# Optimization experiments

Hardware: AMD Instinct MI355X
Metric: run time of the kernel (lower is better)

Reference implementation:

```python
import jax, jax.numpy as jnp
import numpy as np

D_IN = 1024
D_OUT = 1024
NUM_HEAD = 16
HEAD_DIM = D_OUT // NUM_HEAD
CTX = 2048


def setup_inputs() -> dict:
    key = jax.random.key(0)
    ks = jax.random.split(key, 7)
    s = 0.02
    x = jax.random.normal(ks[0], (2, CTX, D_IN), dtype=jnp.float32)
    Wq = jax.random.normal(ks[1], (D_IN, D_OUT), dtype=jnp.float32) * s
    Wk = jax.random.normal(ks[2], (D_IN, D_OUT), dtype=jnp.float32) * s
    Wv = jax.random.normal(ks[3], (D_IN, D_OUT), dtype=jnp.float32) * s
    Wo = jax.random.normal(ks[4], (D_OUT, D_OUT), dtype=jnp.float32) * s
    bo = jax.random.normal(ks[5], (D_OUT,), dtype=jnp.float32) * s
    return {"x": x, "Wq": Wq, "Wk": Wk, "Wv": Wv, "Wo": Wo, "bo": bo}


def reference(x, Wq, Wk, Wv, Wo, bo):
    B, T, _ = x.shape
    # QKV projections, split into heads: [B, H, T, hd]
    def split_heads(y):
        return y.reshape(B, T, NUM_HEAD, HEAD_DIM).transpose(0, 2, 1, 3)
    q = split_heads(x @ Wq)
    k = split_heads(x @ Wk)
    v = split_heads(x @ Wv)
    # scaled causal attention scores [B, H, T, T]
    scores = jnp.einsum("bhqd,bhkd->bhqk", q, k) / jnp.sqrt(
        jnp.asarray(HEAD_DIM, dtype=x.dtype))
    causal = jnp.tril(jnp.ones((T, T), dtype=bool))  # mask buffer triu(diag=1) -> keep lower tri
    scores = jnp.where(causal[None, None], scores, jnp.asarray(-jnp.inf, dtype=x.dtype))
    attn = jax.nn.softmax(scores, axis=-1)
    # dropout with droprate=0.0 is identity
    ctx = jnp.einsum("bhqk,bhkd->bhqd", attn, v)
    ctx = ctx.transpose(0, 2, 1, 3).reshape(B, T, D_OUT)
    return ctx @ Wo + bo
```

## Files before the change

### kernel.cpp

```cpp
#include <hip/hip_runtime.h>

typedef __bf16 bf16x8 __attribute__((ext_vector_type(8)));
typedef float f32x4 __attribute__((ext_vector_type(4)));

__device__ inline float bf2f(unsigned short u) {
    unsigned int x = ((unsigned int)u) << 16;
    return __builtin_bit_cast(float, x);
}
__device__ inline unsigned short f2bf(float f) {
    unsigned int x = __builtin_bit_cast(unsigned int, f);
    x += 0x7fff + ((x >> 16) & 1);
    return (unsigned short)(x >> 16);
}

__device__ __forceinline__ void gl_lds16(const unsigned short* g, unsigned short* l)
{
    __builtin_amdgcn_global_load_lds(
        (const __attribute__((address_space(1))) void*)g,
        (__attribute__((address_space(3))) void*)l, 16, 0, 0);
}

__global__ __launch_bounds__(256)
void prep(const float* __restrict__ x, unsigned short* __restrict__ xb,
          const float* __restrict__ Wq, const float* __restrict__ Wk,
          const float* __restrict__ Wv, unsigned short* __restrict__ wT)
{
    __shared__ unsigned short T[64][72];
    if (blockIdx.x < 2048) {
        const size_t i = ((size_t)blockIdx.x * 256 + threadIdx.x) * 8;
        float4 a = *reinterpret_cast<const float4*>(x + i);
        float4 b = *reinterpret_cast<const float4*>(x + i + 4);
        unsigned short t[8] = { f2bf(a.x), f2bf(a.y), f2bf(a.z), f2bf(a.w),
                                f2bf(b.x), f2bf(b.y), f2bf(b.z), f2bf(b.w) };
        *reinterpret_cast<uint4*>(xb + i) = *reinterpret_cast<uint4*>(t);
        return;
    }
    const int blk = blockIdx.x - 2048;
    const int z = blk >> 8, within = blk & 255;
    const float* W = (z == 0) ? Wq : (z == 1) ? Wk : Wv;
    unsigned short* dstBase = wT + (size_t)z * 1024 * 1024;
    const int k0 = (within >> 4) * 64, n0 = (within & 15) * 64;
    const int r = threadIdx.x >> 2, c0 = (threadIdx.x & 3) * 16;
    const float* src = W + (size_t)(k0 + r) * 1024 + n0 + c0;
    #pragma unroll
    for (int j = 0; j < 16; j += 4) {
        float4 f = *reinterpret_cast<const float4*>(src + j);
        T[r][c0 + j]     = f2bf(f.x);
        T[r][c0 + j + 1] = f2bf(f.y);
        T[r][c0 + j + 2] = f2bf(f.z);
        T[r][c0 + j + 3] = f2bf(f.w);
    }
    __syncthreads();
    unsigned short* dst = dstBase + (size_t)(n0 + r) * 1024 + k0 + c0;
    #pragma unroll
    for (int h = 0; h < 2; ++h) {
        unsigned short t8[8];
        #pragma unroll
        for (int j = 0; j < 8; ++j) t8[j] = T[c0 + h * 8 + j][r];
        *reinterpret_cast<uint4*>(dst + h * 8) = *reinterpret_cast<uint4*>(t8);
    }
}

__global__ __launch_bounds__(256)
void wconv(const float* __restrict__ W, unsigned short* __restrict__ wT)
{
    __shared__ unsigned short T[64][72];
    const int k0 = blockIdx.y * 64, n0 = blockIdx.x * 64;
    const int r = threadIdx.x >> 2, c0 = (threadIdx.x & 3) * 16;
    const float* src = W + (size_t)(k0 + r) * 1024 + n0 + c0;
    #pragma unroll
    for (int j = 0; j < 16; j += 4) {
        float4 f = *reinterpret_cast<const float4*>(src + j);
        T[r][c0 + j]     = f2bf(f.x);
        T[r][c0 + j + 1] = f2bf(f.y);
        T[r][c0 + j + 2] = f2bf(f.z);
        T[r][c0 + j + 3] = f2bf(f.w);
    }
    __syncthreads();
    unsigned short* dst = wT + (size_t)(n0 + r) * 1024 + k0 + c0;
    #pragma unroll
    for (int h = 0; h < 2; ++h) {
        unsigned short t8[8];
        #pragma unroll
        for (int j = 0; j < 8; ++j) t8[j] = T[c0 + h * 8 + j][r];
        *reinterpret_cast<uint4*>(dst + h * 8) = *reinterpret_cast<uint4*>(t8);
    }
}

template <int MODE>
__global__ __launch_bounds__(256)
void gemm128(const unsigned short* __restrict__ A,
             const unsigned short* __restrict__ BT,
             void* __restrict__ C0, void* __restrict__ C1,
             void* __restrict__ C2, const float* __restrict__ bias)
{
    __shared__ unsigned short As[128 * 32];
    __shared__ unsigned short Bs[128 * 32];

    const int tid = threadIdx.x;
    const int wave = tid >> 6, lane = tid & 63, quad = lane >> 4, l16 = lane & 15;
    const int wm = wave >> 1, wn = wave & 1;
    const int mBase = blockIdx.y * 128, nBase = blockIdx.x * 128;

    f32x4 acc[4][4] = {};

    const int srow = lane >> 2, sko = (lane & 3) * 8;

    for (int kb = 0; kb < 1024; kb += 32) {
        __syncthreads();
        #pragma unroll
        for (int j = 0; j < 2; ++j) {
            const int seg = wave * 2 + j;
            gl_lds16(A  + (size_t)(mBase + seg * 16 + srow) * 1024 + kb + sko,
                     As + seg * 512);
            gl_lds16(BT + (size_t)(nBase + seg * 16 + srow) * 1024 + kb + sko,
                     Bs + seg * 512);
        }
        __syncthreads();

        bf16x8 af[4], bf[4];
        #pragma unroll
        for (int t = 0; t < 4; ++t) {
            af[t] = *reinterpret_cast<const bf16x8*>(&As[(wm * 64 + t * 16 + l16) * 32 + quad * 8]);
            bf[t] = *reinterpret_cast<const bf16x8*>(&Bs[(wn * 64 + t * 16 + l16) * 32 + quad * 8]);
        }
        #pragma unroll
        for (int ti = 0; ti < 4; ++ti)
            #pragma unroll
            for (int tj = 0; tj < 4; ++tj)
                acc[ti][tj] = __builtin_amdgcn_mfma_f32_16x16x32_bf16(
                    af[ti], bf[tj], acc[ti][tj], 0, 0, 0);
    }

    #pragma unroll
    for (int ti = 0; ti < 4; ++ti) {
        const int row0 = mBase + wm * 64 + ti * 16 + quad * 4;
        #pragma unroll
        for (int tj = 0; tj < 4; ++tj) {
            const int col = nBase + wn * 64 + tj * 16 + l16;
            if constexpr (MODE == 0) {
                if (col < 1024) {
                    unsigned short* qb = (unsigned short*)C0;
                    #pragma unroll
                    for (int i = 0; i < 4; ++i)
                        qb[(size_t)(row0 + i) * 1024 + col] = f2bf(acc[ti][tj][i]);
                } else if (col < 2048) {
                    unsigned short* kb = (unsigned short*)C1;
                    #pragma unroll
                    for (int i = 0; i < 4; ++i)
                        kb[(size_t)(row0 + i) * 1024 + col - 1024] = f2bf(acc[ti][tj][i]);
                } else {
                    unsigned short* vT = (unsigned short*)C2;
                    unsigned short t4[4] = { f2bf(acc[ti][tj][0]), f2bf(acc[ti][tj][1]),
                                             f2bf(acc[ti][tj][2]), f2bf(acc[ti][tj][3]) };
                    *reinterpret_cast<uint2*>(&vT[(size_t)(col - 2048) * 4096 + row0]) =
                        *reinterpret_cast<uint2*>(t4);
                }
            } else {
                float* out = (float*)C0;
                const float ba = bias[col];
                #pragma unroll
                for (int i = 0; i < 4; ++i)
                    out[(size_t)(row0 + i) * 1024 + col] = acc[ti][tj][i] + ba;
            }
        }
    }
}

#define LDP 72

__global__ __launch_bounds__(256)
void attn6(const unsigned short* __restrict__ q,
           const unsigned short* __restrict__ k,
           const unsigned short* __restrict__ vT,
           unsigned short* __restrict__ ctx)
{
    __shared__ unsigned short Ks[2][2][64 * 32];
    __shared__ unsigned short Vs[2][2][64 * 32];
    __shared__ unsigned short PsA[64 * LDP];
    __shared__ unsigned short PsB[64 * LDP];

    const int tid  = threadIdx.x;
    const int wave = tid >> 6, lane = tid & 63, quad = lane >> 4, l16 = lane & 15;
    const int j  = blockIdx.x;
    const int bh = blockIdx.y;
    const int b = bh >> 4, h = bh & 15;
    const int tokBase = b * 2048;
    const int colBase = h * 64;
    const int qtA = 31 - j, qtB = j;
    const int qBaseA = qtA * 64, qBaseB = qtB * 64;

    bf16x8 aqA[2], aqB[2];
    {
        const unsigned short* qrA =
            q + (size_t)(tokBase + qBaseA + wave * 16 + l16) * 1024 + colBase;
        aqA[0] = *reinterpret_cast<const bf16x8*>(qrA + quad * 8);
        aqA[1] = *reinterpret_cast<const bf16x8*>(qrA + 32 + quad * 8);
        const unsigned short* qrB =
            q + (size_t)(tokBase + qBaseB + wave * 16 + l16) * 1024 + colBase;
        aqB[0] = *reinterpret_cast<const bf16x8*>(qrB + quad * 8);
        aqB[1] = *reinterpret_cast<const bf16x8*>(qrB + 32 + quad * 8);
    }

    f32x4 oA[4] = {}, oB[4] = {};
    float lsA[4] = {}, lsB[4] = {};

    const int sa = lane >> 2;
    const int sb = (lane & 3) * 8;

    auto stage = [&](int tok0, int buf) {
        #pragma unroll
        for (int o = 0; o < 2; ++o) {
            const int op = wave * 2 + o;
            const int hh = op >> 2, rg = op & 3;
            gl_lds16(k + (size_t)(tok0 + rg * 16 + sa) * 1024 + colBase + hh * 32 + sb,
                     &Ks[buf][hh][rg * 16 * 32]);
            gl_lds16(vT + (size_t)(colBase + rg * 16 + sa) * 4096 + tok0 + hh * 32 + sb,
                     &Vs[buf][hh][rg * 16 * 32]);
        }
    };

    stage(tokBase, 0);
    __syncthreads();

    const int nkt = qtA + 1;
    for (int kt = 0; kt < nkt; ++kt) {
        const int buf = kt & 1;
        if (kt + 1 < nkt)
            stage(tokBase + (kt + 1) * 64, buf ^ 1);

        const bool doB = (kt <= qtB);
        const bool diagA = (kt == qtA), diagB = (kt == qtB);

        {
            f32x4 sc[4] = {};
            #pragma unroll
            for (int t = 0; t < 4; ++t)
                #pragma unroll
                for (int kf = 0; kf < 2; ++kf) {
                    bf16x8 bk = *reinterpret_cast<const bf16x8*>(
                        &Ks[buf][kf][(t * 16 + l16) * 32 + quad * 8]);
                    sc[t] = __builtin_amdgcn_mfma_f32_16x16x32_bf16(aqA[kf], bk, sc[t], 0, 0, 0);
                }
            #pragma unroll
            for (int t = 0; t < 4; ++t) {
                const int ki = kt * 64 + t * 16 + l16;
                #pragma unroll
                for (int r = 0; r < 4; ++r) {
                    float p = __expf(sc[t][r] * 0.125f);
                    if (diagA && ki > qBaseA + wave * 16 + quad * 4 + r) p = 0.0f;
                    lsA[r] += p;
                    PsA[(wave * 16 + quad * 4 + r) * LDP + t * 16 + l16] = f2bf(p);
                }
            }
        }
        if (doB) {
            f32x4 sc[4] = {};
            #pragma unroll
            for (int t = 0; t < 4; ++t)
                #pragma unroll
                for (int kf = 0; kf < 2; ++kf) {
                    bf16x8 bk = *reinterpret_cast<const bf16x8*>(
                        &Ks[buf][kf][(t * 16 + l16) * 32 + quad * 8]);
                    sc[t] = __builtin_amdgcn_mfma_f32_16x16x32_bf16(aqB[kf], bk, sc[t], 0, 0, 0);
                }
            #pragma unroll
            for (int t = 0; t < 4; ++t) {
                const int ki = kt * 64 + t * 16 + l16;
                #pragma unroll
                for (int r = 0; r < 4; ++r) {
                    float p = __expf(sc[t][r] * 0.125f);
                    if (diagB && ki > qBaseB + wave * 16 + quad * 4 + r) p = 0.0f;
                    lsB[r] += p;
                    PsB[(wave * 16 + quad * 4 + r) * LDP + t * 16 + l16] = f2bf(p);
                }
            }
        }

        #pragma unroll
        for (int kf = 0; kf < 2; ++kf) {
            if (diagA && (wave * 16 + 15) < kf * 32) continue;
            bf16x8 ap = *reinterpret_cast<const bf16x8*>(
                &PsA[(wave * 16 + l16) * LDP + kf * 32 + quad * 8]);
            #pragma unroll
            for (int t = 0; t < 4; ++t) {
                bf16x8 bv = *reinterpret_cast<const bf16x8*>(
                    &Vs[buf][kf][(t * 16 + l16) * 32 + quad * 8]);
                oA[t] = __builtin_amdgcn_mfma_f32_16x16x32_bf16(ap, bv, oA[t], 0, 0, 0);
            }
        }
        if (doB) {
            #pragma unroll
            for (int kf = 0; kf < 2; ++kf) {
                if (diagB && (wave * 16 + 15) < kf * 32) continue;
                bf16x8 ap = *reinterpret_cast<const bf16x8*>(
                    &PsB[(wave * 16 + l16) * LDP + kf * 32 + quad * 8]);
                #pragma unroll
                for (int t = 0; t < 4; ++t) {
                    bf16x8 bv = *reinterpret_cast<const bf16x8*>(
                        &Vs[buf][kf][(t * 16 + l16) * 32 + quad * 8]);
                    oB[t] = __builtin_amdgcn_mfma_f32_16x16x32_bf16(ap, bv, oB[t], 0, 0, 0);
                }
            }
        }

        if (kt + 1 < nkt)
            __syncthreads();
    }

    #pragma unroll
    for (int off = 1; off < 16; off <<= 1)
        #pragma unroll
        for (int r = 0; r < 4; ++r) {
            lsA[r] += __shfl_xor(lsA[r], off);
            lsB[r] += __shfl_xor(lsB[r], off);
        }

    #pragma unroll
    for (int r = 0; r < 4; ++r) {
        const float invA = 1.0f / lsA[r];
        const float invB = 1.0f / lsB[r];
        const size_t grA = (size_t)(tokBase + qBaseA + wave * 16 + quad * 4 + r) * 1024 + colBase;
        const size_t grB = (size_t)(tokBase + qBaseB + wave * 16 + quad * 4 + r) * 1024 + colBase;
        #pragma unroll
        for (int t = 0; t < 4; ++t) {
            ctx[grA + t * 16 + l16] = f2bf(oA[t][r] * invA);
            ctx[grB + t * 16 + l16] = f2bf(oB[t][r] * invB);
        }
    }
}

extern "C" void kernel_launch(void* const* d_in, const int* in_sizes, int n_in,
                              void* d_out, int out_size, void* d_ws, size_t ws_size,
                              hipStream_t stream)
{
    const float* x  = (const float*)d_in[0];
    const float* Wq = (const float*)d_in[1];
    const float* Wk = (const float*)d_in[2];
    const float* Wv = (const float*)d_in[3];
    const float* Wo = (const float*)d_in[4];
    const float* bo = (const float*)d_in[5];
    float* out = (float*)d_out;

    unsigned short* xb     = (unsigned short*)d_ws;
    unsigned short* qb     = xb + (size_t)4096 * 1024;
    unsigned short* kb     = qb + (size_t)4096 * 1024;
    unsigned short* vT     = kb + (size_t)4096 * 1024;
    unsigned short* ctx    = xb;
    unsigned short* wqkvT  = (unsigned short*)d_out;
    unsigned short* woT    = kb;

    prep<<<2816, 256, 0, stream>>>(x, xb, Wq, Wk, Wv, wqkvT);

    gemm128<0><<<dim3(24, 32), 256, 0, stream>>>(xb, wqkvT, qb, kb, vT, nullptr);

    attn6<<<dim3(16, 32), 256, 0, stream>>>(qb, kb, vT, ctx);

    wconv<<<dim3(16, 16), 256, 0, stream>>>(Wo, woT);

    gemm128<2><<<dim3(8, 32), 256, 0, stream>>>(ctx, woT, out, nullptr, nullptr, bo);
}
```

Before: 194.4 us.

## Double GEMM K-step per barrier, use exp2 softmax and native bf16 conversion

```diff
diff --git a/kernel.cpp b/kernel.cpp
--- a/kernel.cpp
+++ b/kernel.cpp
@@ -3,14 +3,9 @@
 typedef __bf16 bf16x8 __attribute__((ext_vector_type(8)));
 typedef float f32x4 __attribute__((ext_vector_type(4)));
 
-__device__ inline float bf2f(unsigned short u) {
-    unsigned int x = ((unsigned int)u) << 16;
-    return __builtin_bit_cast(float, x);
-}
 __device__ inline unsigned short f2bf(float f) {
-    unsigned int x = __builtin_bit_cast(unsigned int, f);
-    x += 0x7fff + ((x >> 16) & 1);
-    return (unsigned short)(x >> 16);
+    __bf16 b = (__bf16)f;
+    return __builtin_bit_cast(unsigned short, b);
 }
 
 __device__ __forceinline__ void gl_lds16(const unsigned short* g, unsigned short* l)
@@ -94,8 +89,8 @@
              void* __restrict__ C0, void* __restrict__ C1,
              void* __restrict__ C2, const float* __restrict__ bias)
 {
-    __shared__ unsigned short As[128 * 32];
-    __shared__ unsigned short Bs[128 * 32];
+    __shared__ unsigned short As[2][128 * 32];
+    __shared__ unsigned short Bs[2][128 * 32];
 
     const int tid = threadIdx.x;
     const int wave = tid >> 6, lane = tid & 63, quad = lane >> 4, l16 = lane & 15;
@@ -104,32 +99,36 @@
 
     f32x4 acc[4][4] = {};
 
-    const int srow = lane >> 2, sko = (lane & 3) * 8;
-
-    for (int kb = 0; kb < 1024; kb += 32) {
+    const int sa = lane >> 2, sb = (lane & 3) * 8;
+
+    for (int kb = 0; kb < 1024; kb += 64) {
         __syncthreads();
         #pragma unroll
-        for (int j = 0; j < 2; ++j) {
-            const int seg = wave * 2 + j;
-            gl_lds16(A  + (size_t)(mBase + seg * 16 + srow) * 1024 + kb + sko,
-                     As + seg * 512);
-            gl_lds16(BT + (size_t)(nBase + seg * 16 + srow) * 1024 + kb + sko,
-                     Bs + seg * 512);
+        for (int j = 0; j < 4; ++j) {
+            const int op = wave * 4 + j;
+            const int hh = op >> 3, rg = op & 7;
+            gl_lds16(A  + (size_t)(mBase + rg * 16 + sa) * 1024 + kb + hh * 32 + sb,
+                     &As[hh][rg * 512]);
+            gl_lds16(BT + (size_t)(nBase + rg * 16 + sa) * 1024 + kb + hh * 32 + sb,
+                     &Bs[hh][rg * 512]);
         }
         __syncthreads();
 
-        bf16x8 af[4], bf[4];
-        #pragma unroll
-        for (int t = 0; t < 4; ++t) {
-            af[t] = *reinterpret_cast<const bf16x8*>(&As[(wm * 64 + t * 16 + l16) * 32 + quad * 8]);
-            bf[t] = *reinterpret_cast<const bf16x8*>(&Bs[(wn * 64 + t * 16 + l16) * 32 + quad * 8]);
-        }
-        #pragma unroll
-        for (int ti = 0; ti < 4; ++ti)
-            #pragma unroll
-            for (int tj = 0; tj < 4; ++tj)
-                acc[ti][tj] = __builtin_amdgcn_mfma_f32_16x16x32_bf16(
-                    af[ti], bf[tj], acc[ti][tj], 0, 0, 0);
+        #pragma unroll
+        for (int kk = 0; kk < 2; ++kk) {
+            bf16x8 af[4], bf[4];
+            #pragma unroll
+            for (int t = 0; t < 4; ++t) {
+                af[t] = *reinterpret_cast<const bf16x8*>(&As[kk][(wm * 64 + t * 16 + l16) * 32 + quad * 8]);
+                bf[t] = *reinterpret_cast<const bf16x8*>(&Bs[kk][(wn * 64 + t * 16 + l16) * 32 + quad * 8]);
+            }
+            #pragma unroll
+            for (int ti = 0; ti < 4; ++ti)
+                #pragma unroll
+                for (int tj = 0; tj < 4; ++tj)
+                    acc[ti][tj] = __builtin_amdgcn_mfma_f32_16x16x32_bf16(
+                        af[ti], bf[tj], acc[ti][tj], 0, 0, 0);
+        }
     }
 
     #pragma unroll
@@ -168,6 +167,7 @@
 }
 
 #define LDP 72
+#define EXP2_SCL 0.18033688011112042f
 
 __global__ __launch_bounds__(256)
 void attn6(const unsigned short* __restrict__ q,
@@ -247,7 +247,7 @@
                 const int ki = kt * 64 + t * 16 + l16;
                 #pragma unroll
                 for (int r = 0; r < 4; ++r) {
-                    float p = __expf(sc[t][r] * 0.125f);
+                    float p = exp2f(sc[t][r] * EXP2_SCL);
                     if (diagA && ki > qBaseA + wave * 16 + quad * 4 + r) p = 0.0f;
                     lsA[r] += p;
                     PsA[(wave * 16 + quad * 4 + r) * LDP + t * 16 + l16] = f2bf(p);
@@ -269,7 +269,7 @@
                 const int ki = kt * 64 + t * 16 + l16;
                 #pragma unroll
                 for (int r = 0; r < 4; ++r) {
-                    float p = __expf(sc[t][r] * 0.125f);
+                    float p = exp2f(sc[t][r] * EXP2_SCL);
                     if (diagB && ki > qBaseB + wave * 16 + quad * 4 + r) p = 0.0f;
                     lsB[r] += p;
                     PsB[(wave * 16 + quad * 4 + r) * LDP + t * 16 + l16] = f2bf(p);
```

Measured after the change: 207.9 us. 7.0% more time.
